# Optimization experiments

Hardware: AMD Instinct MI355X
Metric: run time of the kernel (lower is better)

Reference implementation:

```python
import jax, jax.numpy as jnp
import numpy as np

B, C, IC, H = 16, 256, 64, 56
EPS = 1e-5
SCALE = float((H * H * C) ** -0.5)


def conv1x1(x, w, b=None):
    # x: [B,Cin,H,W], w: [Cout,Cin]
    y = jnp.einsum('bchw,oc->bohw', x, w)
    return y if b is None else y + b[None, :, None, None]


def bn_eval(x, g, be):
    # eval-mode BatchNorm2d with running_mean=0, running_var=1
    s = g / np.float32(np.sqrt(1.0 + EPS))
    return x * s[None, :, None, None] + be[None, :, None, None]


def lrelu(x):
    return jnp.where(x >= 0, x, 0.2 * x)


def setup_inputs() -> dict:
    key = jax.random.key(0)
    ks = jax.random.split(key, 16)
    def w(i, shape, s=0.05):
        return jax.random.normal(ks[i], shape, jnp.float32) * s
    return {
        'x_s': w(0, (B, C, H, H), 1.0),
        'x_fq': w(1, (B, C, H, H), 1.0),
        'x_mt': w(2, (B, C, H, H), 1.0),
        # local_att: conv(C->IC)+BN+LReLU+conv(IC->C)+BN
        'la_w1': w(3, (IC, C)), 'la_b1': jnp.zeros(IC, jnp.float32),
        'la_g1': jnp.ones(IC, jnp.float32), 'la_be1': jnp.zeros(IC, jnp.float32),
        'la_w2': w(4, (C, IC)), 'la_b2': jnp.zeros(C, jnp.float32),
        'la_g2': jnp.ones(C, jnp.float32), 'la_be2': jnp.zeros(C, jnp.float32),
        'lk_w': w(5, (C, C)), 'lk_b': jnp.zeros(C, jnp.float32),
        'lv_w': w(6, (C, C)),  # l_convv has bias=False
        # global_att (after avg-pool): conv+BN+LReLU+conv+BN
        'ga_w1': w(7, (IC, C)), 'ga_b1': jnp.zeros(IC, jnp.float32),
        'ga_g1': jnp.ones(IC, jnp.float32), 'ga_be1': jnp.zeros(IC, jnp.float32),
        'ga_w2': w(8, (C, IC)), 'ga_b2': jnp.zeros(C, jnp.float32),
        'ga_g2': jnp.ones(C, jnp.float32), 'ga_be2': jnp.zeros(C, jnp.float32),
        'gk_w': w(9, (C, C)), 'gk_b': jnp.zeros(C, jnp.float32),
        'gv_w': w(10, (C, C)),  # convv has bias=False
        'c11_w': w(11, (C, C)), 'c11_b': jnp.zeros(C, jnp.float32),
        'c1_w': w(12, (C, C)), 'c1_b': jnp.zeros(C, jnp.float32),
    }


def reference(x_s, x_fq, x_mt,
              la_w1, la_b1, la_g1, la_be1, la_w2, la_b2, la_g2, la_be2,
              lk_w, lk_b, lv_w,
              ga_w1, ga_b1, ga_g1, ga_be1, ga_w2, ga_b2, ga_g2, ga_be2,
              gk_w, gk_b, gv_w, c11_w, c11_b, c1_w, c1_b):
    # ---- local branch ----
    l_q = bn_eval(conv1x1(lrelu(bn_eval(conv1x1(x_s, la_w1, la_b1), la_g1, la_be1)),
                          la_w2, la_b2), la_g2, la_be2)
    l_k = conv1x1(x_s, lk_w, lk_b)
    l_v = conv1x1(x_s, lv_w)
    # l_q @ l_k^T over the spatial matrix of each (b,c): [H,W]@[W,H]->[H,H]
    att = jax.nn.softmax(jnp.einsum('bchw,bcvw->bchv', l_q, l_k) * SCALE, axis=-1)
    l_fuse = jnp.einsum('bchv,bcvw->bchw', att, l_v)  # [B,C,H,W]
    # ---- global branch ----
    p = jnp.mean(conv1x1(x_mt, c11_w, c11_b), axis=(2, 3), keepdims=True)  # [B,C,1,1]
    g_q = bn_eval(conv1x1(lrelu(bn_eval(conv1x1(p, ga_w1, ga_b1), ga_g1, ga_be1)),
                          ga_w2, ga_b2), ga_g2, ga_be2)  # [B,C,1,1]
    g_k = conv1x1(x_fq, gk_w, gk_b)
    g_v = conv1x1(x_fq, gv_w)
    gatt = jax.nn.softmax(g_q * g_k * SCALE, axis=-1)  # softmax over W
    g_fuse = jnp.einsum('bchk,bckw->bchw', gatt, g_v)  # requires H==W (square maps)
    # ---- output conv: kernel 1 with padding 1 -> spatial grows to H+2 ----
    f = jnp.pad(l_fuse + g_fuse, ((0, 0), (0, 0), (1, 1), (1, 1)))
    return conv1x1(f, c1_w, c1_b)  # [B,C,H+2,W+2]
```

## Files before the change

### kernel.cpp

```cpp
#include <hip/hip_runtime.h>
#include <hip/hip_bf16.h>

typedef __bf16 bf16;
typedef __bf16 bf16x8 __attribute__((ext_vector_type(8)));
typedef float  f32x4  __attribute__((ext_vector_type(4)));

#define S_SP 3136
#define SCALE_V (1.0f/896.0f)

__device__ __forceinline__ float bf2f(bf16 x) { return (float)x; }

__device__ __forceinline__ bf16x8 load8(const float* p) {
    f32x4 a = *(const f32x4*)p;
    f32x4 b = *(const f32x4*)(p + 4);
    bf16x8 r;
    r[0] = (bf16)a[0]; r[1] = (bf16)a[1]; r[2] = (bf16)a[2]; r[3] = (bf16)a[3];
    r[4] = (bf16)b[0]; r[5] = (bf16)b[1]; r[6] = (bf16)b[2]; r[7] = (bf16)b[3];
    return r;
}
__device__ __forceinline__ bf16x8 load8(const bf16* p) { return *(const bf16x8*)p; }

template<typename T> struct raw8;
template<> struct raw8<float> { f32x4 a, b; };
template<> struct raw8<bf16>  { bf16x8 v; };
__device__ __forceinline__ raw8<float> loadraw(const float* p) {
    return { *(const f32x4*)p, *(const f32x4*)(p + 4) };
}
__device__ __forceinline__ raw8<bf16> loadraw(const bf16* p) {
    return { *(const bf16x8*)p };
}
__device__ __forceinline__ bf16 elem8(const raw8<float>& r, int u) {
    return (bf16)(u < 4 ? r.a[u] : r.b[u - 4]);
}
__device__ __forceinline__ bf16 elem8(const raw8<bf16>& r, int u) { return r.v[u]; }

template<int NSEC>
__global__ __launch_bounds__(256)
void conv_multi_kernel(const float* __restrict__ X,
                       const float* __restrict__ Wa, const float* __restrict__ ba,
                       bf16* __restrict__ Ya,
                       const float* __restrict__ Wb, bf16* __restrict__ Yb,
                       const float* __restrict__ Wc, const float* __restrict__ bc,
                       const float* __restrict__ gc, const float* __restrict__ bec,
                       bf16* __restrict__ Yc)
{
    __shared__ bf16 Xt[2][64][72];
    const int wg  = blockIdx.x;
    const int xcd = wg & 7;
    const int idx = wg >> 3;
    const int sec = idx % NSEC;
    const int t   = idx / NSEC;
    const int tile = xcd * 98 + t;
    const int s0  = (tile % 49) * 64;
    const int b   = tile / 49;
    const int tid = threadIdx.x;
    const int wv = tid >> 6, lane = tid & 63, li = lane & 15, quad = lane >> 4;

    const float* Xb = X + (size_t)b * 256 * S_SP;

    const float* W; const float* bias = nullptr;
    const float* bng = nullptr; const float* bnb = nullptr;
    bf16* Y; int o0, O; bool two, lrelu = false;
    if (sec < 2)      { W = Wa; bias = ba; Y = Ya; o0 = sec * 128;       two = true;  O = 256; }
    else if (sec < 4) { W = Wb;            Y = Yb; o0 = (sec - 2) * 128; two = true;  O = 256; }
    else              { W = Wc; bias = bc; bng = gc; bnb = bec; Y = Yc;
                        o0 = 0; two = false; lrelu = true; O = 64; }

    f32x4 acc[2][4];
    #pragma unroll
    for (int mt = 0; mt < 2; ++mt)
        #pragma unroll
        for (int nt = 0; nt < 4; ++nt) acc[mt][nt] = f32x4{0.f, 0.f, 0.f, 0.f};

    const int cl  = tid >> 3;
    const int sj  = (tid & 7) * 8;
    const int g   = cl >> 3;
    const int clo = cl & 7;
    const float* xp = Xb + (size_t)cl * S_SP + s0 + sj;

    raw8<float> v = loadraw(xp);
    int p = 0;
    #pragma unroll
    for (int k0 = 0; k0 < 256; k0 += 32) {
        #pragma unroll
        for (int u = 0; u < 8; ++u) {
            int r  = sj + u;
            int gp = g ^ ((r >> 3) & 3);
            Xt[p][r][gp * 8 + clo] = elem8(v, u);
        }
        raw8<float> vn = v;
        if (k0 + 32 < 256) vn = loadraw(xp + (size_t)(k0 + 32) * S_SP);
        __syncthreads();
        bf16x8 a0 = load8(W + (size_t)(o0 + wv * 16 + li) * 256 + k0 + quad * 8);
        bf16x8 a1;
        if (two) a1 = load8(W + (size_t)(o0 + 64 + wv * 16 + li) * 256 + k0 + quad * 8);
        #pragma unroll
        for (int nt = 0; nt < 4; ++nt) {
            int row = nt * 16 + li;
            int gp  = quad ^ ((row >> 3) & 3);
            bf16x8 bb = *(const bf16x8*)&Xt[p][row][gp * 8];
            acc[0][nt] = __builtin_amdgcn_mfma_f32_16x16x32_bf16(a0, bb, acc[0][nt], 0, 0, 0);
            if (two)
                acc[1][nt] = __builtin_amdgcn_mfma_f32_16x16x32_bf16(a1, bb, acc[1][nt], 0, 0, 0);
        }
        v = vn;
        p ^= 1;
    }

    const float rs = rsqrtf(1.0f + 1e-5f);
    const int nm = two ? 2 : 1;
    for (int mt = 0; mt < nm; ++mt) {
        #pragma unroll
        for (int r = 0; r < 4; ++r) {
            int o = o0 + mt * 64 + wv * 16 + quad * 4 + r;
            float bi = bias ? bias[o] : 0.f;
            float sc = bng ? bng[o] * rs : 1.f;
            float sh = bnb ? bnb[o] : 0.f;
            #pragma unroll
            for (int nt = 0; nt < 4; ++nt) {
                float val = acc[mt][nt][r] + bi;
                val = val * sc + sh;
                if (lrelu) val = (val >= 0.f) ? val : 0.2f * val;
                int s = s0 + nt * 16 + li;
                Y[((size_t)b * O + o) * S_SP + s] = (bf16)val;
            }
        }
    }
}

template<typename TX, typename TY, int CIN, int MT, int NSEC, bool LRELU, bool PAD_OUT>
__global__ __launch_bounds__(256)
void conv1x1_kernel(const TX* __restrict__ X, const float* __restrict__ W,
                    const float* __restrict__ bias, const float* __restrict__ bng,
                    const float* __restrict__ bnb, TY* __restrict__ Y, int O)
{
    __shared__ bf16 Xt[2][64][72];
    const int wg  = blockIdx.x;
    const int xcd = wg & 7;
    const int idx = wg >> 3;
    const int sec = idx % NSEC;
    const int t   = idx / NSEC;
    const int tile = xcd * 98 + t;
    const int s0  = (tile % 49) * 64;
    const int b   = tile / 49;
    const int o0  = sec * (MT * 64);
    const int tid = threadIdx.x;
    const int wv = tid >> 6, lane = tid & 63, li = lane & 15, quad = lane >> 4;

    const TX* Xb = X + (size_t)b * CIN * S_SP;

    f32x4 acc[MT][4];
    #pragma unroll
    for (int mt = 0; mt < MT; ++mt)
        #pragma unroll
        for (int nt = 0; nt < 4; ++nt) acc[mt][nt] = f32x4{0.f, 0.f, 0.f, 0.f};

    const int cl  = tid >> 3;
    const int sj  = (tid & 7) * 8;
    const int g   = cl >> 3;
    const int clo = cl & 7;
    const TX* xp = Xb + (size_t)cl * S_SP + s0 + sj;

    raw8<TX> v = loadraw(xp);
    int p = 0;
    #pragma unroll
    for (int k0 = 0; k0 < CIN; k0 += 32) {
        #pragma unroll
        for (int u = 0; u < 8; ++u) {
            int r  = sj + u;
            int gp = g ^ ((r >> 3) & 3);
            Xt[p][r][gp * 8 + clo] = elem8(v, u);
        }
        raw8<TX> vn = v;
        if (k0 + 32 < CIN) vn = loadraw(xp + (size_t)(k0 + 32) * S_SP);
        __syncthreads();
        bf16x8 a[MT];
        #pragma unroll
        for (int mt = 0; mt < MT; ++mt)
            a[mt] = load8(W + (size_t)(o0 + mt * 64 + wv * 16 + li) * CIN + k0 + quad * 8);
        #pragma unroll
        for (int nt = 0; nt < 4; ++nt) {
            int row = nt * 16 + li;
            int gp  = quad ^ ((row >> 3) & 3);
            bf16x8 bb = *(const bf16x8*)&Xt[p][row][gp * 8];
            #pragma unroll
            for (int mt = 0; mt < MT; ++mt)
                acc[mt][nt] = __builtin_amdgcn_mfma_f32_16x16x32_bf16(a[mt], bb, acc[mt][nt], 0, 0, 0);
        }
        v = vn;
        p ^= 1;
    }

    const float rs = rsqrtf(1.0f + 1e-5f);
    #pragma unroll
    for (int mt = 0; mt < MT; ++mt) {
        #pragma unroll
        for (int r = 0; r < 4; ++r) {
            int o = o0 + mt * 64 + wv * 16 + quad * 4 + r;
            float bi = bias ? bias[o] : 0.f;
            float sc = bng ? bng[o] * rs : 1.f;
            float sh = bnb ? bnb[o] : 0.f;
            #pragma unroll
            for (int nt = 0; nt < 4; ++nt) {
                float val = acc[mt][nt][r] + bi;
                val = val * sc + sh;
                if (LRELU) val = (val >= 0.f) ? val : 0.2f * val;
                int s = s0 + nt * 16 + li;
                if (!PAD_OUT) {
                    Y[((size_t)b * O + o) * S_SP + s] = (TY)val;
                } else {
                    int rr = s / 56, cc = s % 56;
                    Y[(((size_t)b * O + o) * 58 + rr + 1) * 58 + cc + 1] = (TY)val;
                }
            }
        }
    }
}

__global__ __launch_bounds__(256)
void attn_kernel(const bf16* __restrict__ Q, const bf16* __restrict__ K,
                 const bf16* __restrict__ V, const float* __restrict__ gq,
                 const bf16* __restrict__ GK, const bf16* __restrict__ GV,
                 bf16* __restrict__ F)
{
    __shared__ bf16 Qs[64][72], Ks[64][72], Vt[64][72], Ps[64][72];
    const int bc  = blockIdx.x;
    const int tid = threadIdx.x;
    const int wv = tid >> 6, lane = tid & 63, li = lane & 15, quad = lane >> 4;
    const int m0 = wv * 16;

    #pragma unroll
    for (int i = tid; i < 64 * 36; i += 256) {
        ((uint32_t*)Qs)[i] = 0; ((uint32_t*)Ks)[i] = 0;
        ((uint32_t*)Vt)[i] = 0; ((uint32_t*)Ps)[i] = 0;
    }
    __syncthreads();

    const bf16* Qp = Q + (size_t)bc * S_SP;
    const bf16* Kp = K + (size_t)bc * S_SP;
    const bf16* Vp = V + (size_t)bc * S_SP;
    for (int idx = tid; idx < 392; idx += 256) {
        int r = idx / 7, cj = (idx % 7) * 8;
        *(bf16x8*)&Qs[r][cj] = *(const bf16x8*)(Qp + r * 56 + cj);
        *(bf16x8*)&Ks[r][cj] = *(const bf16x8*)(Kp + r * 56 + cj);
        bf16x8 vv = *(const bf16x8*)(Vp + r * 56 + cj);
        int q = r >> 3, rlo = r & 7;
        #pragma unroll
        for (int u = 0; u < 8; ++u) {
            int row = cj + u;
            int gp  = q ^ ((row >> 3) & 3);
            Vt[row][gp * 8 + rlo] = vv[u];
        }
    }

    const float gs = gq[bc];
    const bf16* GVp = GV + (size_t)bc * S_SP;
    const bf16* GKp = GK + (size_t)bc * S_SP;
    const int ra  = tid / 7,            cja = (tid % 7) * 8;
    const bool hasb = tid < 136;
    const int rb  = (tid + 256) / 7,    cjb = ((tid + 256) % 7) * 8;
    bf16x8 gva = *(const bf16x8*)(GVp + ra * 56 + cja);
    bf16x8 gvb = hasb ? *(const bf16x8*)(GVp + rb * 56 + cjb) : bf16x8{};
    __syncthreads();

    f32x4 sacc[4];
    #pragma unroll
    for (int nt = 0; nt < 4; ++nt) sacc[nt] = f32x4{0.f, 0.f, 0.f, 0.f};
    #pragma unroll
    for (int k0 = 0; k0 < 64; k0 += 32) {
        bf16x8 a = *(const bf16x8*)&Qs[m0 + li][k0 + quad * 8];
        #pragma unroll
        for (int nt = 0; nt < 4; ++nt) {
            bf16x8 bb = *(const bf16x8*)&Ks[nt * 16 + li][k0 + quad * 8];
            sacc[nt] = __builtin_amdgcn_mfma_f32_16x16x32_bf16(a, bb, sacc[nt], 0, 0, 0);
        }
    }

    #pragma unroll
    for (int r = 0; r < 4; ++r) {
        float e[4]; float m = -3e38f;
        #pragma unroll
        for (int nt = 0; nt < 4; ++nt) {
            int v = nt * 16 + li;
            float x = (v < 56) ? sacc[nt][r] * SCALE_V : -3e38f;
            e[nt] = x; m = fmaxf(m, x);
        }
        m = fmaxf(m, __shfl_xor(m, 1)); m = fmaxf(m, __shfl_xor(m, 2));
        m = fmaxf(m, __shfl_xor(m, 4)); m = fmaxf(m, __shfl_xor(m, 8));
        float s = 0.f;
        #pragma unroll
        for (int nt = 0; nt < 4; ++nt) {
            float pp = (nt * 16 + li < 56) ? __expf(e[nt] - m) : 0.f;
            e[nt] = pp; s += pp;
        }
        s += __shfl_xor(s, 1); s += __shfl_xor(s, 2);
        s += __shfl_xor(s, 4); s += __shfl_xor(s, 8);
        float inv = 1.f / s;
        int row = m0 + quad * 4 + r;
        #pragma unroll
        for (int nt = 0; nt < 4; ++nt) Ps[row][nt * 16 + li] = (bf16)(e[nt] * inv);
    }

    float gkv[4][4];
    #pragma unroll
    for (int r = 0; r < 4; ++r) {
        int row = m0 + quad * 4 + r;
        int hrow = (row < 56) ? row : 0;
        #pragma unroll
        for (int nt = 0; nt < 4; ++nt) {
            int v = nt * 16 + li;
            gkv[r][nt] = (v < 56) ? bf2f(GKp[hrow * 56 + v]) : 0.f;
        }
    }
    __syncthreads();

    f32x4 oacc[4];
    #pragma unroll
    for (int nt = 0; nt < 4; ++nt) oacc[nt] = f32x4{0.f, 0.f, 0.f, 0.f};
    #pragma unroll
    for (int k0 = 0; k0 < 64; k0 += 32) {
        bf16x8 a = *(const bf16x8*)&Ps[m0 + li][k0 + quad * 8];
        int kq = (k0 >> 3) + quad;
        #pragma unroll
        for (int nt = 0; nt < 4; ++nt) {
            int row = nt * 16 + li;
            int gp  = kq ^ ((row >> 3) & 3);
            bf16x8 bb = *(const bf16x8*)&Vt[row][gp * 8];
            oacc[nt] = __builtin_amdgcn_mfma_f32_16x16x32_bf16(a, bb, oacc[nt], 0, 0, 0);
        }
    }

    __syncthreads();

    {
        int q = ra >> 3, rlo = ra & 7;
        #pragma unroll
        for (int u = 0; u < 8; ++u) {
            int row = cja + u;
            int gp  = q ^ ((row >> 3) & 3);
            Vt[row][gp * 8 + rlo] = gva[u];
        }
        if (hasb) {
            int qb = rb >> 3, rblo = rb & 7;
            #pragma unroll
            for (int u = 0; u < 8; ++u) {
                int row = cjb + u;
                int gp  = qb ^ ((row >> 3) & 3);
                Vt[row][gp * 8 + rblo] = gvb[u];
            }
        }
    }

    #pragma unroll
    for (int r = 0; r < 4; ++r) {
        float e[4]; float m = -3e38f;
        #pragma unroll
        for (int nt = 0; nt < 4; ++nt) {
            int v = nt * 16 + li;
            float x = (v < 56) ? gs * gkv[r][nt] : -3e38f;
            e[nt] = x; m = fmaxf(m, x);
        }
        m = fmaxf(m, __shfl_xor(m, 1)); m = fmaxf(m, __shfl_xor(m, 2));
        m = fmaxf(m, __shfl_xor(m, 4)); m = fmaxf(m, __shfl_xor(m, 8));
        float s = 0.f;
        #pragma unroll
        for (int nt = 0; nt < 4; ++nt) {
            float pp = (nt * 16 + li < 56) ? __expf(e[nt] - m) : 0.f;
            e[nt] = pp; s += pp;
        }
        s += __shfl_xor(s, 1); s += __shfl_xor(s, 2);
        s += __shfl_xor(s, 4); s += __shfl_xor(s, 8);
        float inv = 1.f / s;
        int row = m0 + quad * 4 + r;
        #pragma unroll
        for (int nt = 0; nt < 4; ++nt) Ps[row][nt * 16 + li] = (bf16)(e[nt] * inv);
    }
    __syncthreads();

    #pragma unroll
    for (int k0 = 0; k0 < 64; k0 += 32) {
        bf16x8 a = *(const bf16x8*)&Ps[m0 + li][k0 + quad * 8];
        int kq = (k0 >> 3) + quad;
        #pragma unroll
        for (int nt = 0; nt < 4; ++nt) {
            int row = nt * 16 + li;
            int gp  = kq ^ ((row >> 3) & 3);
            bf16x8 bb = *(const bf16x8*)&Vt[row][gp * 8];
            oacc[nt] = __builtin_amdgcn_mfma_f32_16x16x32_bf16(a, bb, oacc[nt], 0, 0, 0);
        }
    }

    bf16* Fp = F + (size_t)bc * S_SP;
    #pragma unroll
    for (int r = 0; r < 4; ++r) {
        int h = m0 + quad * 4 + r;
        #pragma unroll
        for (int nt = 0; nt < 4; ++nt) {
            int w = nt * 16 + li;
            if (h < 56 && w < 56) Fp[h * 56 + w] = (bf16)oacc[nt][r];
        }
    }
}

__global__ __launch_bounds__(256)
void spatial_mean_kernel(const float* __restrict__ X, float* __restrict__ out)
{
    int bc = blockIdx.x, tid = threadIdx.x;
    const float* p = X + (size_t)bc * S_SP;
    float s = 0.f;
    for (int i = tid; i < S_SP; i += 256) s += p[i];
    for (int off = 32; off; off >>= 1) s += __shfl_down(s, off, 64);
    __shared__ float ws[4];
    if ((tid & 63) == 0) ws[tid >> 6] = s;
    __syncthreads();
    if (tid == 0) out[bc] = (ws[0] + ws[1] + ws[2] + ws[3]) * (1.0f / S_SP);
}

__global__ __launch_bounds__(256)
void gq_kernel(const float* __restrict__ pmean,
               const float* c11w, const float* c11b,
               const float* gaw1, const float* gab1, const float* gag1, const float* gabe1,
               const float* gaw2, const float* gab2, const float* gag2, const float* gabe2,
               float* __restrict__ gq)
{
    __shared__ float pm[256], p2[256], hh[64];
    int b = blockIdx.x, t = threadIdx.x;
    pm[t] = pmean[b * 256 + t];
    __syncthreads();
    float a = c11b[t];
    for (int c = 0; c < 256; ++c) a += c11w[t * 256 + c] * pm[c];
    p2[t] = a;
    __syncthreads();
    const float rs = rsqrtf(1.0f + 1e-5f);
    if (t < 64) {
        float h = gab1[t];
        for (int c = 0; c < 256; ++c) h += gaw1[t * 256 + c] * p2[c];
        h = h * (gag1[t] * rs) + gabe1[t];
        hh[t] = (h >= 0.f) ? h : 0.2f * h;
    }
    __syncthreads();
    float g = gab2[t];
    for (int i = 0; i < 64; ++i) g += gaw2[t * 64 + i] * hh[i];
    g = g * (gag2[t] * rs) + gabe2[t];
    gq[b * 256 + t] = g * SCALE_V;
}

__global__ __launch_bounds__(256)
void fill_border_kernel(float* __restrict__ out, const float* __restrict__ c1b)
{
    int idx = blockIdx.x * 256 + threadIdx.x;
    int e  = idx % 228;
    int bo = idx / 228;
    if (bo >= 16 * 256) return;
    int o = bo & 255;
    int r, c;
    if (e < 58)       { r = 0;  c = e; }
    else if (e < 116) { r = 57; c = e - 58; }
    else { int t = e - 116; r = 1 + (t >> 1); c = (t & 1) * 57; }
    out[(size_t)bo * 3364 + r * 58 + c] = c1b[o];
}

extern "C" void kernel_launch(void* const* d_in, const int* in_sizes, int n_in,
                              void* d_out, int out_size, void* d_ws, size_t ws_size,
                              hipStream_t stream)
{
    (void)in_sizes; (void)n_in; (void)out_size; (void)ws_size;
    const float* x_s   = (const float*)d_in[0];
    const float* x_fq  = (const float*)d_in[1];
    const float* x_mt  = (const float*)d_in[2];
    const float* la_w1 = (const float*)d_in[3];
    const float* la_b1 = (const float*)d_in[4];
    const float* la_g1 = (const float*)d_in[5];
    const float* la_be1= (const float*)d_in[6];
    const float* la_w2 = (const float*)d_in[7];
    const float* la_b2 = (const float*)d_in[8];
    const float* la_g2 = (const float*)d_in[9];
    const float* la_be2= (const float*)d_in[10];
    const float* lk_w  = (const float*)d_in[11];
    const float* lk_b  = (const float*)d_in[12];
    const float* lv_w  = (const float*)d_in[13];
    const float* ga_w1 = (const float*)d_in[14];
    const float* ga_b1 = (const float*)d_in[15];
    const float* ga_g1 = (const float*)d_in[16];
    const float* ga_be1= (const float*)d_in[17];
    const float* ga_w2 = (const float*)d_in[18];
    const float* ga_b2 = (const float*)d_in[19];
    const float* ga_g2 = (const float*)d_in[20];
    const float* ga_be2= (const float*)d_in[21];
    const float* gk_w  = (const float*)d_in[22];
    const float* gk_b  = (const float*)d_in[23];
    const float* gv_w  = (const float*)d_in[24];
    const float* c11_w = (const float*)d_in[25];
    const float* c11_b = (const float*)d_in[26];
    const float* c1_w  = (const float*)d_in[27];
    const float* c1_b  = (const float*)d_in[28];
    float* out = (float*)d_out;

    char* ws = (char*)d_ws;
    const size_t SZ = (size_t)16 * 256 * S_SP * 2;
    bf16* Q  = (bf16*)(ws);
    bf16* K  = (bf16*)(ws + SZ);
    bf16* V  = (bf16*)(ws + 2 * SZ);
    bf16* GK = (bf16*)(ws + 3 * SZ);
    bf16* GV = (bf16*)(ws + 4 * SZ);
    bf16* Hd = (bf16*)(ws + 5 * SZ);
    float* pmean = (float*)(ws + 5 * SZ + (size_t)16 * 64 * S_SP * 2);
    float* gq    = pmean + 16 * 256;
    bf16* F  = Q;

    dim3 blk(256);
    fill_border_kernel<<<dim3(3648), blk, 0, stream>>>(out, c1_b);

    conv_multi_kernel<5><<<dim3(8 * 98 * 5), blk, 0, stream>>>(
        x_s, lk_w, lk_b, K, lv_w, V,
        la_w1, la_b1, la_g1, la_be1, Hd);
    conv1x1_kernel<bf16, bf16, 64, 2, 2, false, false><<<dim3(8 * 98 * 2), blk, 0, stream>>>(
        Hd, la_w2, la_b2, la_g2, la_be2, Q, 256);

    spatial_mean_kernel<<<dim3(4096), blk, 0, stream>>>(x_mt, pmean);
    gq_kernel<<<dim3(16), blk, 0, stream>>>(pmean, c11_w, c11_b,
        ga_w1, ga_b1, ga_g1, ga_be1, ga_w2, ga_b2, ga_g2, ga_be2, gq);
    conv_multi_kernel<4><<<dim3(8 * 98 * 4), blk, 0, stream>>>(
        x_fq, gk_w, gk_b, GK, gv_w, GV,
        nullptr, nullptr, nullptr, nullptr, nullptr);

    attn_kernel<<<dim3(4096), blk, 0, stream>>>(Q, K, V, gq, GK, GV, F);

    conv1x1_kernel<bf16, float, 256, 2, 2, false, true><<<dim3(8 * 98 * 2), blk, 0, stream>>>(
        F, c1_w, c1_b, nullptr, nullptr, out, 256);
}
```

Measured before the change: 497.0 us.

## Pre-convert weights to bf16, merge projection convs, preload all X tiles into registers

Adds a small kernel that converts all 1x1 conv weights to bf16 once per call, so the GEMM kernels load bf16 weights directly instead of converting fp32 on every tile. The x_s and x_fq projection convs are merged into a single 9-section launch. Inside the conv kernels, all K-slices of the input column are loaded into registers up front, and the next weight fragment is prefetched while LDS is double-buffered. This is meant to cut load latency and launch count, at the cost of higher register pressure (8 bf16x8 input registers per thread) and one extra launch.

```diff
diff --git a/kernel.cpp b/kernel.cpp
--- a/kernel.cpp
+++ b/kernel.cpp
@@ -7,6 +7,15 @@
 
 #define S_SP 3136
 #define SCALE_V (1.0f/896.0f)
+
+#define OFF_LK   0
+#define OFF_LV   65536
+#define OFF_LA1  131072
+#define OFF_GK   147456
+#define OFF_GV   212992
+#define OFF_LA2  278528
+#define OFF_C1   294912
+#define WTOT     360448
 
 __device__ __forceinline__ float bf2f(bf16 x) { return (float)x; }
 
@@ -20,80 +29,100 @@
 }
 __device__ __forceinline__ bf16x8 load8(const bf16* p) { return *(const bf16x8*)p; }
 
-template<typename T> struct raw8;
-template<> struct raw8<float> { f32x4 a, b; };
-template<> struct raw8<bf16>  { bf16x8 v; };
-__device__ __forceinline__ raw8<float> loadraw(const float* p) {
-    return { *(const f32x4*)p, *(const f32x4*)(p + 4) };
-}
-__device__ __forceinline__ raw8<bf16> loadraw(const bf16* p) {
-    return { *(const bf16x8*)p };
-}
-__device__ __forceinline__ bf16 elem8(const raw8<float>& r, int u) {
-    return (bf16)(u < 4 ? r.a[u] : r.b[u - 4]);
-}
-__device__ __forceinline__ bf16 elem8(const raw8<bf16>& r, int u) { return r.v[u]; }
-
-template<int NSEC>
-__global__ __launch_bounds__(256)
-void conv_multi_kernel(const float* __restrict__ X,
-                       const float* __restrict__ Wa, const float* __restrict__ ba,
-                       bf16* __restrict__ Ya,
-                       const float* __restrict__ Wb, bf16* __restrict__ Yb,
-                       const float* __restrict__ Wc, const float* __restrict__ bc,
-                       const float* __restrict__ gc, const float* __restrict__ bec,
-                       bf16* __restrict__ Yc)
+__global__ __launch_bounds__(256)
+void wprep_kernel(const float* __restrict__ lk, const float* __restrict__ lv,
+                  const float* __restrict__ la1, const float* __restrict__ gk,
+                  const float* __restrict__ gv, const float* __restrict__ la2,
+                  const float* __restrict__ c1, bf16* __restrict__ dst)
+{
+    int i = blockIdx.x * 256 + threadIdx.x;
+    const float* s; int off;
+    if      (i < OFF_LV)  { s = lk;  off = i; }
+    else if (i < OFF_LA1) { s = lv;  off = i - OFF_LV; }
+    else if (i < OFF_GK)  { s = la1; off = i - OFF_LA1; }
+    else if (i < OFF_GV)  { s = gk;  off = i - OFF_GK; }
+    else if (i < OFF_LA2) { s = gv;  off = i - OFF_GV; }
+    else if (i < OFF_C1)  { s = la2; off = i - OFF_LA2; }
+    else                  { s = c1;  off = i - OFF_C1; }
+    dst[i] = (bf16)s[off];
+}
+
+__global__ __launch_bounds__(256)
+void conv_multi_kernel(const float* __restrict__ xs, const float* __restrict__ xfq,
+                       const bf16* __restrict__ Wbf,
+                       const float* __restrict__ lk_b,
+                       const float* __restrict__ la_b1, const float* __restrict__ la_g1,
+                       const float* __restrict__ la_be1,
+                       const float* __restrict__ gk_b,
+                       bf16* __restrict__ K, bf16* __restrict__ V, bf16* __restrict__ Hd,
+                       bf16* __restrict__ GK, bf16* __restrict__ GV)
 {
     __shared__ bf16 Xt[2][64][72];
     const int wg  = blockIdx.x;
     const int xcd = wg & 7;
     const int idx = wg >> 3;
-    const int sec = idx % NSEC;
-    const int t   = idx / NSEC;
+    const int sec = idx % 9;
+    const int t   = idx / 9;
     const int tile = xcd * 98 + t;
     const int s0  = (tile % 49) * 64;
     const int b   = tile / 49;
     const int tid = threadIdx.x;
     const int wv = tid >> 6, lane = tid & 63, li = lane & 15, quad = lane >> 4;
 
-    const float* Xb = X + (size_t)b * 256 * S_SP;
-
-    const float* W; const float* bias = nullptr;
-    const float* bng = nullptr; const float* bnb = nullptr;
-    bf16* Y; int o0, O; bool two, lrelu = false;
-    if (sec < 2)      { W = Wa; bias = ba; Y = Ya; o0 = sec * 128;       two = true;  O = 256; }
-    else if (sec < 4) { W = Wb;            Y = Yb; o0 = (sec - 2) * 128; two = true;  O = 256; }
-    else              { W = Wc; bias = bc; bng = gc; bnb = bec; Y = Yc;
-                        o0 = 0; two = false; lrelu = true; O = 64; }
-
-    f32x4 acc[2][4];
-    #pragma unroll
-    for (int mt = 0; mt < 2; ++mt)
-        #pragma unroll
-        for (int nt = 0; nt < 4; ++nt) acc[mt][nt] = f32x4{0.f, 0.f, 0.f, 0.f};
+    const float* X; const bf16* W;
+    const float* bias = nullptr; const float* bng = nullptr; const float* bnb = nullptr;
+    bf16* Y; int o0 = 0, O = 256; bool two = true, lrelu = false;
+    if (sec < 2)      { X = xs;  W = Wbf + OFF_LK; bias = lk_b; Y = K;  o0 = sec * 128; }
+    else if (sec < 4) { X = xs;  W = Wbf + OFF_LV;              Y = V;  o0 = (sec - 2) * 128; }
+    else if (sec == 4){ X = xs;  W = Wbf + OFF_LA1; bias = la_b1; bng = la_g1; bnb = la_be1;
+                        Y = Hd; O = 64; two = false; lrelu = true; }
+    else if (sec < 7) { X = xfq; W = Wbf + OFF_GK; bias = gk_b; Y = GK; o0 = (sec - 5) * 128; }
+    else              { X = xfq; W = Wbf + OFF_GV;              Y = GV; o0 = (sec - 7) * 128; }
 
     const int cl  = tid >> 3;
     const int sj  = (tid & 7) * 8;
     const int g   = cl >> 3;
     const int clo = cl & 7;
-    const float* xp = Xb + (size_t)cl * S_SP + s0 + sj;
-
-    raw8<float> v = loadraw(xp);
+
+    const float* xp = X + (size_t)b * 256 * S_SP + (size_t)cl * S_SP + s0 + sj;
+    bf16x8 xr[8];
+    #pragma unroll
+    for (int i = 0; i < 8; ++i) xr[i] = load8(xp + (size_t)i * 32 * S_SP);
+
+    f32x4 acc[2][4];
+    #pragma unroll
+    for (int mt = 0; mt < 2; ++mt)
+        #pragma unroll
+        for (int nt = 0; nt < 4; ++nt) acc[mt][nt] = f32x4{0.f, 0.f, 0.f, 0.f};
+
+    const bf16* wp0 = W + (size_t)(o0 + wv * 16 + li) * 256 + quad * 8;
+    const bf16* wp1 = W + (size_t)(o0 + 64 + wv * 16 + li) * 256 + quad * 8;
+    bf16x8 a0 = *(const bf16x8*)wp0;
+    bf16x8 a1{};
+    if (two) a1 = *(const bf16x8*)wp1;
+
+    #pragma unroll
+    for (int u = 0; u < 8; ++u) {
+        int r = sj + u;
+        int gp = g ^ ((r >> 3) & 3);
+        Xt[0][r][gp * 8 + clo] = xr[0][u];
+    }
+    __syncthreads();
+
     int p = 0;
     #pragma unroll
-    for (int k0 = 0; k0 < 256; k0 += 32) {
-        #pragma unroll
-        for (int u = 0; u < 8; ++u) {
-            int r  = sj + u;
-            int gp = g ^ ((r >> 3) & 3);
-            Xt[p][r][gp * 8 + clo] = elem8(v, u);
-        }
-        raw8<float> vn = v;
-        if (k0 + 32 < 256) vn = loadraw(xp + (size_t)(k0 + 32) * S_SP);
-        __syncthreads();
-        bf16x8 a0 = load8(W + (size_t)(o0 + wv * 16 + li) * 256 + k0 + quad * 8);
-        bf16x8 a1;
-        if (two) a1 = load8(W + (size_t)(o0 + 64 + wv * 16 + li) * 256 + k0 + quad * 8);
+    for (int k = 0; k < 8; ++k) {
+        bf16x8 na0{}, na1{};
+        if (k + 1 < 8) {
+            na0 = *(const bf16x8*)(wp0 + (k + 1) * 32);
+            if (two) na1 = *(const bf16x8*)(wp1 + (k + 1) * 32);
+            #pragma unroll
+            for (int u = 0; u < 8; ++u) {
+                int r = sj + u;
+                int gp = g ^ ((r >> 3) & 3);
+                Xt[p ^ 1][r][gp * 8 + clo] = xr[k + 1][u];
+            }
+        }
         #pragma unroll
         for (int nt = 0; nt < 4; ++nt) {
             int row = nt * 16 + li;
@@ -103,8 +132,8 @@
             if (two)
                 acc[1][nt] = __builtin_amdgcn_mfma_f32_16x16x32_bf16(a1, bb, acc[1][nt], 0, 0, 0);
         }
-        v = vn;
-        p ^= 1;
+        __syncthreads();
+        a0 = na0; a1 = na1; p ^= 1;
     }
 
     const float rs = rsqrtf(1.0f + 1e-5f);
@@ -128,12 +157,13 @@
     }
 }
 
-template<typename TX, typename TY, int CIN, int MT, int NSEC, bool LRELU, bool PAD_OUT>
-__global__ __launch_bounds__(256)
-void conv1x1_kernel(const TX* __restrict__ X, const float* __restrict__ W,
+template<typename TY, int CIN, int NSEC, bool LRELU, bool PAD_OUT>
+__global__ __launch_bounds__(256)
+void conv1x1_kernel(const bf16* __restrict__ X, const bf16* __restrict__ W,
                     const float* __restrict__ bias, const float* __restrict__ bng,
                     const float* __restrict__ bnb, TY* __restrict__ Y, int O)
 {
+    constexpr int NS = CIN / 32;
     __shared__ bf16 Xt[2][64][72];
     const int wg  = blockIdx.x;
     const int xcd = wg & 7;
@@ -143,57 +173,68 @@
     const int tile = xcd * 98 + t;
     const int s0  = (tile % 49) * 64;
     const int b   = tile / 49;
-    const int o0  = sec * (MT * 64);
+    const int o0  = sec * 128;
     const int tid = threadIdx.x;
     const int wv = tid >> 6, lane = tid & 63, li = lane & 15, quad = lane >> 4;
-
-    const TX* Xb = X + (size_t)b * CIN * S_SP;
-
-    f32x4 acc[MT][4];
-    #pragma unroll
-    for (int mt = 0; mt < MT; ++mt)
-        #pragma unroll
-        for (int nt = 0; nt < 4; ++nt) acc[mt][nt] = f32x4{0.f, 0.f, 0.f, 0.f};
 
     const int cl  = tid >> 3;
     const int sj  = (tid & 7) * 8;
     const int g   = cl >> 3;
     const int clo = cl & 7;
-    const TX* xp = Xb + (size_t)cl * S_SP + s0 + sj;
-
-    raw8<TX> v = loadraw(xp);
+
+    const bf16* xp = X + (size_t)b * CIN * S_SP + (size_t)cl * S_SP + s0 + sj;
+    bf16x8 xr[NS];
+    #pragma unroll
+    for (int i = 0; i < NS; ++i) xr[i] = load8(xp + (size_t)i * 32 * S_SP);
+
+    f32x4 acc[2][4];
+    #pragma unroll
+    for (int mt = 0; mt < 2; ++mt)
+        #pragma unroll
+        for (int nt = 0; nt < 4; ++nt) acc[mt][nt] = f32x4{0.f, 0.f, 0.f, 0.f};
+
+    const bf16* wp0 = W + (size_t)(o0 + wv * 16 + li) * CIN + quad * 8;
+    const bf16* wp1 = W + (size_t)(o0 + 64 + wv * 16 + li) * CIN + quad * 8;
+    bf16x8 a0 = *(const bf16x8*)wp0;
+    bf16x8 a1 = *(const bf16x8*)wp1;
+
+    #pragma unroll
+    for (int u = 0; u < 8; ++u) {
+        int r = sj + u;
+        int gp = g ^ ((r >> 3) & 3);
+        Xt[0][r][gp * 8 + clo] = xr[0][u];
+    }
+    __syncthreads();
+
     int p = 0;
     #pragma unroll
-    for (int k0 = 0; k0 < CIN; k0 += 32) {
-        #pragma unroll
-        for (int u = 0; u < 8; ++u) {
-            int r  = sj + u;
-            int gp = g ^ ((r >> 3) & 3);
-            Xt[p][r][gp * 8 + clo] = elem8(v, u);
-        }
-        raw8<TX> vn = v;
-        if (k0 + 32 < CIN) vn = loadraw(xp + (size_t)(k0 + 32) * S_SP);
-        __syncthreads();
-        bf16x8 a[MT];
-        #pragma unroll
-        for (int mt = 0; mt < MT; ++mt)
-            a[mt] = load8(W + (size_t)(o0 + mt * 64 + wv * 16 + li) * CIN + k0 + quad * 8);
+    for (int k = 0; k < NS; ++k) {
+        bf16x8 na0{}, na1{};
+        if (k + 1 < NS) {
+            na0 = *(const bf16x8*)(wp0 + (k + 1) * 32);
+            na1 = *(const bf16x8*)(wp1 + (k + 1) * 32);
+            #pragma unroll
+            for (int u = 0; u < 8; ++u) {
+                int r = sj + u;
+                int gp = g ^ ((r >> 3) & 3);
+                Xt[p ^ 1][r][gp * 8 + clo] = xr[k + 1][u];
+            }
+        }
         #pragma unroll
         for (int nt = 0; nt < 4; ++nt) {
             int row = nt * 16 + li;
             int gp  = quad ^ ((row >> 3) & 3);
             bf16x8 bb = *(const bf16x8*)&Xt[p][row][gp * 8];
-            #pragma unroll
-            for (int mt = 0; mt < MT; ++mt)
-                acc[mt][nt] = __builtin_amdgcn_mfma_f32_16x16x32_bf16(a[mt], bb, acc[mt][nt], 0, 0, 0);
-        }
-        v = vn;
-        p ^= 1;
+            acc[0][nt] = __builtin_amdgcn_mfma_f32_16x16x32_bf16(a0, bb, acc[0][nt], 0, 0, 0);
+            acc[1][nt] = __builtin_amdgcn_mfma_f32_16x16x32_bf16(a1, bb, acc[1][nt], 0, 0, 0);
+        }
+        __syncthreads();
+        a0 = na0; a1 = na1; p ^= 1;
     }
 
     const float rs = rsqrtf(1.0f + 1e-5f);
     #pragma unroll
-    for (int mt = 0; mt < MT; ++mt) {
+    for (int mt = 0; mt < 2; ++mt) {
         #pragma unroll
         for (int r = 0; r < 4; ++r) {
             int o = o0 + mt * 64 + wv * 16 + quad * 4 + r;
@@ -506,26 +547,28 @@
     bf16* Hd = (bf16*)(ws + 5 * SZ);
     float* pmean = (float*)(ws + 5 * SZ + (size_t)16 * 64 * S_SP * 2);
     float* gq    = pmean + 16 * 256;
+    bf16* Wbf   = (bf16*)(gq + 16 * 256);
     bf16* F  = Q;
 
     dim3 blk(256);
+    wprep_kernel<<<dim3(1408), blk, 0, stream>>>(
+        lk_w, lv_w, la_w1, gk_w, gv_w, la_w2, c1_w, Wbf);
+
     fill_border_kernel<<<dim3(3648), blk, 0, stream>>>(out, c1_b);
-
-    conv_multi_kernel<5><<<dim3(8 * 98 * 5), blk, 0, stream>>>(
-        x_s, lk_w, lk_b, K, lv_w, V,
-        la_w1, la_b1, la_g1, la_be1, Hd);
-    conv1x1_kernel<bf16, bf16, 64, 2, 2, false, false><<<dim3(8 * 98 * 2), blk, 0, stream>>>(
-        Hd, la_w2, la_b2, la_g2, la_be2, Q, 256);
 
     spatial_mean_kernel<<<dim3(4096), blk, 0, stream>>>(x_mt, pmean);
     gq_kernel<<<dim3(16), blk, 0, stream>>>(pmean, c11_w, c11_b,
         ga_w1, ga_b1, ga_g1, ga_be1, ga_w2, ga_b2, ga_g2, ga_be2, gq);
-    conv_multi_kernel<4><<<dim3(8 * 98 * 4), blk, 0, stream>>>(
-        x_fq, gk_w, gk_b, GK, gv_w, GV,
-        nullptr, nullptr, nullptr, nullptr, nullptr);
+
+    conv_multi_kernel<<<dim3(8 * 98 * 9), blk, 0, stream>>>(
+        x_s, x_fq, Wbf, lk_b, la_b1, la_g1, la_be1, gk_b,
+        K, V, Hd, GK, GV);
+
+    conv1x1_kernel<bf16, 64, 2, false, false><<<dim3(8 * 98 * 2), blk, 0, stream>>>(
+        Hd, Wbf + OFF_LA2, la_b2, la_g2, la_be2, Q, 256);
 
     attn_kernel<<<dim3(4096), blk, 0, stream>>>(Q, K, V, gq, GK, GV, F);
 
-    conv1x1_kernel<bf16, float, 256, 2, 2, false, true><<<dim3(8 * 98 * 2), blk, 0, stream>>>(
-        F, c1_w, c1_b, nullptr, nullptr, out, 256);
-}
+    conv1x1_kernel<float, 256, 2, false, true><<<dim3(8 * 98 * 2), blk, 0, stream>>>(
+        F, Wbf + OFF_C1, c1_b, nullptr, nullptr, out, 256);
+}
```

After: 442.4 us. 1.12x faster.
